# Performance work log

Measured on AMD Instinct MI355X. Metric: run time of the kernel, lower is better.

The kernel has to match this reference:

```python
import jax, jax.numpy as jnp
import numpy as np

N, E, D_IN, D_OUT = 100000, 3200000, 128, 128


def setup_inputs() -> dict:
    key = jax.random.key(0)
    ks = jax.random.split(key, 6)
    return {
        "x": jax.random.normal(ks[0], (N, D_IN), dtype=jnp.float32),
        "row": jax.random.randint(ks[1], (E,), 0, N),
        "col": jax.random.randint(ks[2], (E,), 0, N),
        "W0": jax.random.normal(ks[3], (D_OUT, D_IN), dtype=jnp.float32) * (1.0 / np.sqrt(D_IN)),
        "b0": jnp.zeros((D_OUT,), jnp.float32),
        "W1": jax.random.normal(ks[4], (D_OUT, D_IN), dtype=jnp.float32) * (1.0 / np.sqrt(D_IN)),
        "b1": jnp.zeros((D_OUT,), jnp.float32),
        "att": jax.random.normal(ks[5], (2 * D_OUT,), dtype=jnp.float32) * 0.1,
        "scale0": jnp.ones((D_OUT,), jnp.float32),
        "offset0": jnp.zeros((D_OUT,), jnp.float32),
        "scale1": jnp.ones((D_OUT,), jnp.float32),
        "offset1": jnp.zeros((D_OUT,), jnp.float32),
    }


def _norm(f, scale, offset):
    # per-node normalization over feature dim (bias='norm' branch)
    m = jnp.mean(f, axis=1, keepdims=True)
    v = jnp.var(f, axis=1, keepdims=True) + 1e-9
    return (f - m) * scale * jax.lax.rsqrt(v) + offset


def reference(x, row, col, W0, b0, W1, b1, att, scale0, offset0, scale1, offset1):
    d = W0.shape[0]
    # order-0 (self) and order-1 (neighbor) feature transforms, act='relu'
    h0 = jax.nn.relu(x @ W0.T + b0)  # [N, d]
    h1 = jax.nn.relu(x @ W1.T + b1)  # [N, d]
    # unnormalized GAT attention (no softmax), LeakyReLU(0.2)
    a_self = jax.nn.leaky_relu(h0 @ att[:d], negative_slope=0.2)   # [N]
    a_neigh = jax.nn.leaky_relu(h1 @ att[d:], negative_slope=0.2)  # [N]
    e = a_self[row] + a_neigh[col]                                 # [E]
    # SpMM: out[i] = sum_{(i,j) in edges} e_ij * h1[j]
    agg = jax.ops.segment_sum(e[:, None] * h1[col], row, num_segments=h0.shape[0])
    # batch-norm style normalization per head, then mean-aggregate over orders
    out = _norm(h0, scale0, offset0) + _norm(agg, scale1, offset1)
    return out
```

## Files before the change

### kernel.cpp

```cpp
#include <hip/hip_runtime.h>
#include <hip/hip_bf16.h>

constexpr int D = 128;
constexpr int BUCKET_SHIFT = 6;
constexpr int BUCKET_CAP_LOG2 = 12;
constexpr int BUCKET_CAP = 1 << BUCKET_CAP_LOG2;
constexpr int SEG_SHIFT = 13;
constexpr int NSEG = 13;
constexpr int BINS_PER_BUCKET = 4 * NSEG * 16;
constexpr int BINS_PER_WAVE = NSEG * 16;
constexpr int ROWSTRIDE = 130;
typedef __hip_bfloat16 bf16;
typedef __attribute__((ext_vector_type(8))) short bf16x8;
typedef __attribute__((ext_vector_type(4))) float f32x4;

__device__ __forceinline__ short f2b(float f) {
  bf16 h = __float2bfloat16(f);
  return *reinterpret_cast<short*>(&h);
}

__global__ void k_cvtW(const float* __restrict__ W0, const float* __restrict__ W1,
                       short* __restrict__ Wb0, short* __restrict__ Wb1)
{
  int i = blockIdx.x * 256 + threadIdx.x;
  if (i < 16384) Wb0[i] = f2b(W0[i]);
  else if (i < 32768) { int j = i - 16384; Wb1[j] = f2b(W1[j]); }
}

__global__ __launch_bounds__(256) void k_gemm(
    const float* __restrict__ x,
    const short* __restrict__ Wb0, const float* __restrict__ b0,
    const short* __restrict__ Wb1, const float* __restrict__ b1,
    const float* __restrict__ att,
    float* __restrict__ h0, bf16* __restrict__ h1b,
    float* __restrict__ a_self, float* __restrict__ a_neigh, int N)
{
  const int t = threadIdx.x;
  const int wv = t >> 6;
  const int l = t & 63;
  const int fb = blockIdx.y;
  const int nbase = blockIdx.x * 64 + wv * 16;
  const int lm = l & 15;
  const int lk = l >> 4;

  const short* __restrict__ W    = fb ? Wb1 : Wb0;
  const float* __restrict__ bias = fb ? b1 : b0;
  const float* __restrict__ attp = att + fb * 128;

  f32x4 acc[8];
#pragma unroll
  for (int i = 0; i < 8; ++i) acc[i] = (f32x4){0.f, 0.f, 0.f, 0.f};

  const int node_a = nbase + lm;
  const bool okA = node_a < N;
  const float* xrow = x + (size_t)node_a * D + lk * 8;

#pragma unroll
  for (int ks = 0; ks < 4; ++ks) {
    float4 a0, a1;
    if (okA) {
      a0 = *reinterpret_cast<const float4*>(xrow + ks * 32);
      a1 = *reinterpret_cast<const float4*>(xrow + ks * 32 + 4);
    } else {
      a0 = make_float4(0.f, 0.f, 0.f, 0.f);
      a1 = a0;
    }
    bf16x8 af;
    af[0] = f2b(a0.x); af[1] = f2b(a0.y); af[2] = f2b(a0.z); af[3] = f2b(a0.w);
    af[4] = f2b(a1.x); af[5] = f2b(a1.y); af[6] = f2b(a1.z); af[7] = f2b(a1.w);
#pragma unroll
    for (int nt = 0; nt < 8; ++nt) {
      const bf16x8 bfr = *reinterpret_cast<const bf16x8*>(
          W + (size_t)(nt * 16 + lm) * D + ks * 32 + lk * 8);
      acc[nt] = __builtin_amdgcn_mfma_f32_16x16x32_bf16(af, bfr, acc[nt], 0, 0, 0);
    }
  }

  float pd[4] = {0.f, 0.f, 0.f, 0.f};
#pragma unroll
  for (int nt = 0; nt < 8; ++nt) {
    const int f = nt * 16 + lm;
    const float bv = bias[f];
    const float av = attp[f];
#pragma unroll
    for (int j = 0; j < 4; ++j) {
      const float r = fmaxf(acc[nt][j] + bv, 0.f);
      pd[j] = fmaf(r, av, pd[j]);
      const int ng = nbase + lk * 4 + j;
      if (ng < N) {
        if (fb == 0) h0[(size_t)ng * D + f] = r;
        else         h1b[(size_t)ng * D + f] = __float2bfloat16(r);
      }
    }
  }
#pragma unroll
  for (int m2 = 1; m2 < 16; m2 <<= 1) {
    pd[0] += __shfl_xor(pd[0], m2, 16);
    pd[1] += __shfl_xor(pd[1], m2, 16);
    pd[2] += __shfl_xor(pd[2], m2, 16);
    pd[3] += __shfl_xor(pd[3], m2, 16);
  }
  if (lm == 0) {
    float* __restrict__ adest = fb ? a_neigh : a_self;
#pragma unroll
    for (int j = 0; j < 4; ++j) {
      const int ng = nbase + lk * 4 + j;
      if (ng < N) adest[ng] = pd[j];
    }
  }
}

__global__ __launch_bounds__(512) void k_binA(
    const int* __restrict__ row, const int* __restrict__ col,
    int* __restrict__ bukCnt, unsigned* __restrict__ buf1, int E, int NBUK)
{
  constexpr int EPB = 16384;
  __shared__ int hist[1600];
  __shared__ int base[1600];
  const int t = threadIdx.x;
  const int e0 = blockIdx.x * EPB;
  const int e1 = min(e0 + EPB, E);

  for (int i = t; i < NBUK; i += 512) hist[i] = 0;
  __syncthreads();
  for (int e = e0 + t; e < e1; e += 512)
    atomicAdd(&hist[row[e] >> BUCKET_SHIFT], 1);
  __syncthreads();
  for (int bk = t; bk < NBUK; bk += 512) {
    int c = hist[bk];
    base[bk] = (c > 0) ? atomicAdd(&bukCnt[bk], c) : 0;
  }
  __syncthreads();
  for (int i = t; i < NBUK; i += 512) hist[i] = 0;
  __syncthreads();
  for (int e = e0 + t; e < e1; e += 512) {
    int r = row[e];
    int c = col[e];
    int bk = r >> BUCKET_SHIFT;
    int pos = base[bk] + atomicAdd(&hist[bk], 1);
    if (pos < BUCKET_CAP)
      buf1[((size_t)bk << BUCKET_CAP_LOG2) + pos] =
          ((unsigned)c << BUCKET_SHIFT) | (unsigned)(r & 63);
  }
}

__global__ __launch_bounds__(256) void k_fine(
    const unsigned* __restrict__ buf1,
    const int* __restrict__ bukCnt,
    const float* __restrict__ a_self, const float* __restrict__ a_neigh,
    int* __restrict__ runsW, int2* __restrict__ colS2, int N)
{
  __shared__ int lhist[BINS_PER_BUCKET], labs[BINS_PER_BUCKET], lcur[BINS_PER_BUCKET];
  __shared__ unsigned eL[BUCKET_CAP];
  __shared__ float asF[64];
  __shared__ int sd[256];
  __shared__ int gbS;
  const int b = blockIdx.x;
  const int t = threadIdx.x;
  const int n = min(bukCnt[b], BUCKET_CAP);
  const unsigned* src = buf1 + ((size_t)b << BUCKET_CAP_LOG2);
  const int rstart = b << BUCKET_SHIFT;

  int pre = 0;
  for (int i = t; i < b; i += 256) pre += min(bukCnt[i], BUCKET_CAP);
  sd[t] = pre;
  __syncthreads();
  for (int d2 = 128; d2 > 0; d2 >>= 1) {
    if (t < d2) sd[t] += sd[t + d2];
    __syncthreads();
  }
  if (t == 0) gbS = sd[0];

  for (int i = t; i < BINS_PER_BUCKET; i += 256) { lhist[i] = 0; lcur[i] = 0; }
  if (t < 64) {
    float v = (rstart + t < N) ? a_self[rstart + t] : 0.f;
    asF[t] = v > 0.f ? v : 0.2f * v;
  }
  __syncthreads();
  const int gb = gbS;

  for (int i = t; i < n; i += 256) {
    unsigned e = src[i];
    eL[i] = e;
    int r = e & 63, c = e >> BUCKET_SHIFT;
    int bin = (((r >> 4) * NSEG) + (c >> SEG_SHIFT)) * 16 + (r & 15);
    atomicAdd(&lhist[bin], 1);
  }
  __syncthreads();
  int v[4], s = 0;
  const int bin0 = t * 4;
#pragma unroll
  for (int i = 0; i < 4; ++i) {
    v[i] = (bin0 + i < BINS_PER_BUCKET) ? lhist[bin0 + i] : 0;
    s += v[i];
  }
  sd[t] = s;
  __syncthreads();
  for (int d2 = 1; d2 < 256; d2 <<= 1) {
    int o = (t >= d2) ? sd[t - d2] : 0;
    __syncthreads();
    sd[t] += o;
    __syncthreads();
  }
  int excl = sd[t] - s;
#pragma unroll
  for (int i = 0; i < 4; ++i) {
    if (bin0 + i < BINS_PER_BUCKET) labs[bin0 + i] = gb + excl;
    excl += v[i];
  }
  __syncthreads();
  if (t < 4) runsW[b * 5 + t] = labs[t * BINS_PER_WAVE];
  else if (t == 4) runsW[b * 5 + 4] = gb + n;
  for (int i = t; i < n; i += 256) {
    unsigned e = eL[i];
    int r = e & 63, c = e >> BUCKET_SHIFT;
    int bin = (((r >> 4) * NSEG) + (c >> SEG_SHIFT)) * 16 + (r & 15);
    int pos = labs[bin] + atomicAdd(&lcur[bin], 1);
    float an = a_neigh[c];
    an = an > 0.f ? an : 0.2f * an;
    colS2[pos] = make_int2((c << 8) | r, __float_as_int(asF[r] + an));
  }
}

__global__ __launch_bounds__(128) void k_agg(
    const float* __restrict__ h0, const bf16* __restrict__ h1b,
    const int* __restrict__ runsW, const int2* __restrict__ colS2,
    const float* __restrict__ scale0, const float* __restrict__ offset0,
    const float* __restrict__ scale1, const float* __restrict__ offset1,
    float* __restrict__ out, int N)
{
  __shared__ float aggL[32 * ROWSTRIDE];
  __shared__ int wb[3];
  const int b2 = blockIdx.x;
  const int bk = b2 >> 1, h = b2 & 1;
  const int t = threadIdx.x;
  const int w = t >> 6, l = t & 63;
  const int rbase = (bk << 6) + (h << 5);

  for (int i = t; i < 32 * ROWSTRIDE; i += 128) aggL[i] = 0.f;
  if (t < 3) wb[t] = runsW[bk * 5 + h * 2 + t];
  __syncthreads();

  const char* h1c = reinterpret_cast<const char*>(h1b) + l * 4;
  float acc0 = 0.f, acc1 = 0.f;
  int curRow = -1;

  auto flush = [&]() {
    float* pp = &aggL[(curRow & 31) * ROWSTRIDE + 2 * l];
    const float2 o = *reinterpret_cast<const float2*>(pp);
    *reinterpret_cast<float2*>(pp) = make_float2(o.x + acc0, o.y + acc1);
  };
  auto proc = [&](int2 q, unsigned u) {
    const int r_ = q.x & 63;
    if (r_ != curRow) {
      if (curRow >= 0) flush();
      acc0 = 0.f; acc1 = 0.f; curRow = r_;
    }
    const float wg = __int_as_float(q.y);
    acc0 = fmaf(wg, __uint_as_float(u << 16), acc0);
    acc1 = fmaf(wg, __uint_as_float(u & 0xffff0000u), acc1);
  };
  auto ld = [&](int2 q) -> unsigned {
    return *reinterpret_cast<const unsigned*>(
        h1c + (size_t)((unsigned)q.x & 0xFFFFFF00u));
  };

  const int wbeg = __builtin_amdgcn_readfirstlane(wb[w]);
  const int wend = __builtin_amdgcn_readfirstlane(wb[w + 1]);

  int k = wbeg;
  for (; k + 16 <= wend; k += 16) {
    int2 q[16]; unsigned u[16];
#pragma unroll
    for (int i = 0; i < 16; ++i) q[i] = colS2[k + i];
#pragma unroll
    for (int i = 0; i < 16; ++i) u[i] = ld(q[i]);
#pragma unroll
    for (int i = 0; i < 16; ++i) proc(q[i], u[i]);
  }
  for (; k + 4 <= wend; k += 4) {
    int2 q[4]; unsigned u[4];
#pragma unroll
    for (int i = 0; i < 4; ++i) q[i] = colS2[k + i];
#pragma unroll
    for (int i = 0; i < 4; ++i) u[i] = ld(q[i]);
#pragma unroll
    for (int i = 0; i < 4; ++i) proc(q[i], u[i]);
  }
  for (; k < wend; ++k) {
    const int2 q = colS2[k];
    proc(q, ld(q));
  }
  if (curRow >= 0) flush();
  __syncthreads();

  const float2 sc0 = *reinterpret_cast<const float2*>(&scale0[2 * l]);
  const float2 of0 = *reinterpret_cast<const float2*>(&offset0[2 * l]);
  const float2 sc1 = *reinterpret_cast<const float2*>(&scale1[2 * l]);
  const float2 of1 = *reinterpret_cast<const float2*>(&offset1[2 * l]);
  const float inv = 1.0f / 128.0f;
  for (int i = 0; i < 16; ++i) {
    const int rl = (w << 4) + i;
    const int node = rbase + rl;
    if (node >= N) break;
    const float2 hv = *reinterpret_cast<const float2*>(&h0[(size_t)node * D + 2 * l]);
    const float2 av = *reinterpret_cast<const float2*>(&aggL[rl * ROWSTRIDE + 2 * l]);
    float sh = hv.x + hv.y, qh = hv.x * hv.x + hv.y * hv.y;
    float sa = av.x + av.y, qa = av.x * av.x + av.y * av.y;
#pragma unroll
    for (int o = 32; o; o >>= 1) {
      sh += __shfl_xor(sh, o, 64); qh += __shfl_xor(qh, o, 64);
      sa += __shfl_xor(sa, o, 64); qa += __shfl_xor(qa, o, 64);
    }
    const float m0 = sh * inv, v0 = qh * inv - m0 * m0 + 1e-9f;
    const float m1 = sa * inv, v1 = qa * inv - m1 * m1 + 1e-9f;
    const float r0 = rsqrtf(v0), r1 = rsqrtf(v1);
    float2 o2;
    o2.x = (hv.x - m0) * sc0.x * r0 + of0.x + (av.x - m1) * sc1.x * r1 + of1.x;
    o2.y = (hv.y - m0) * sc0.y * r0 + of0.y + (av.y - m1) * sc1.y * r1 + of1.y;
    *reinterpret_cast<float2*>(&out[(size_t)node * D + 2 * l]) = o2;
  }
}

extern "C" void kernel_launch(void* const* d_in, const int* in_sizes, int n_in,
                              void* d_out, int out_size, void* d_ws, size_t ws_size,
                              hipStream_t stream)
{
  const float* x       = (const float*)d_in[0];
  const int*   row     = (const int*)d_in[1];
  const int*   col     = (const int*)d_in[2];
  const float* W0      = (const float*)d_in[3];
  const float* b0      = (const float*)d_in[4];
  const float* W1      = (const float*)d_in[5];
  const float* b1      = (const float*)d_in[6];
  const float* att     = (const float*)d_in[7];
  const float* scale0  = (const float*)d_in[8];
  const float* offset0 = (const float*)d_in[9];
  const float* scale1  = (const float*)d_in[10];
  const float* offset1 = (const float*)d_in[11];

  const int N = in_sizes[0] / D;
  const int E = in_sizes[1];
  const int NBUK = (N + 63) >> BUCKET_SHIFT;

  char* ws = (char*)d_ws;
  size_t off = 0;
  auto alloc = [&](size_t bytes) -> void* {
    void* p = ws + off;
    off += (bytes + 511) & ~size_t(511);
    return p;
  };

  float*    h0      = (float*)d_out;
  bf16*     h1b     = (bf16*)alloc((size_t)N * D * sizeof(bf16));
  float*    a_self  = (float*)alloc((size_t)N * sizeof(float));
  float*    a_neigh = (float*)alloc((size_t)N * sizeof(float));
  short*    Wb0     = (short*)alloc(16384 * sizeof(short));
  short*    Wb1     = (short*)alloc(16384 * sizeof(short));
  int*      bukCnt  = (int*)alloc((size_t)NBUK * sizeof(int));
  int*      runsW   = (int*)alloc((size_t)NBUK * 5 * sizeof(int));
  unsigned* buf1    = (unsigned*)alloc(((size_t)NBUK << BUCKET_CAP_LOG2) * sizeof(unsigned));
  int2*     colS2   = (int2*)alloc((size_t)E * sizeof(int2));

  hipMemsetAsync(bukCnt, 0, (size_t)NBUK * sizeof(int), stream);

  k_cvtW<<<128, 256, 0, stream>>>(W0, W1, Wb0, Wb1);
  dim3 ggrid((N + 63) / 64, 2);
  k_gemm<<<ggrid, 256, 0, stream>>>(x, Wb0, b0, Wb1, b1, att, h0, h1b,
                                    a_self, a_neigh, N);
  const int NBLKA = (E + 16383) / 16384;
  k_binA<<<NBLKA, 512, 0, stream>>>(row, col, bukCnt, buf1, E, NBUK);
  k_fine<<<NBUK, 256, 0, stream>>>(buf1, bukCnt, a_self, a_neigh,
                                   runsW, colS2, N);
  k_agg<<<NBUK * 2, 128, 0, stream>>>(h0, h1b, runsW, colS2,
                                      scale0, offset0, scale1, offset1,
                                      (float*)d_out, N);
}
```

Baseline: 280.2 us.

## Fuse GEMM and edge-binning into one launch, inline weight bf16 conversion

```diff
diff --git a/kernel.cpp b/kernel.cpp
--- a/kernel.cpp
+++ b/kernel.cpp
@@ -10,6 +10,7 @@
 constexpr int BINS_PER_BUCKET = 4 * NSEG * 16;
 constexpr int BINS_PER_WAVE = NSEG * 16;
 constexpr int ROWSTRIDE = 130;
+constexpr int EPB_BIN = 8192;
 typedef __hip_bfloat16 bf16;
 typedef __attribute__((ext_vector_type(8))) short bf16x8;
 typedef __attribute__((ext_vector_type(4))) float f32x4;
@@ -19,128 +20,125 @@
   return *reinterpret_cast<short*>(&h);
 }
 
-__global__ void k_cvtW(const float* __restrict__ W0, const float* __restrict__ W1,
-                       short* __restrict__ Wb0, short* __restrict__ Wb1)
-{
-  int i = blockIdx.x * 256 + threadIdx.x;
-  if (i < 16384) Wb0[i] = f2b(W0[i]);
-  else if (i < 32768) { int j = i - 16384; Wb1[j] = f2b(W1[j]); }
-}
-
-__global__ __launch_bounds__(256) void k_gemm(
+__global__ __launch_bounds__(256) void k_gb(
     const float* __restrict__ x,
-    const short* __restrict__ Wb0, const float* __restrict__ b0,
-    const short* __restrict__ Wb1, const float* __restrict__ b1,
+    const float* __restrict__ W0, const float* __restrict__ b0,
+    const float* __restrict__ W1, const float* __restrict__ b1,
     const float* __restrict__ att,
     float* __restrict__ h0, bf16* __restrict__ h1b,
-    float* __restrict__ a_self, float* __restrict__ a_neigh, int N)
+    float* __restrict__ a_self, float* __restrict__ a_neigh,
+    const int* __restrict__ row, const int* __restrict__ col,
+    int* __restrict__ bukCnt, unsigned* __restrict__ buf1,
+    int N, int E, int NBUK, int NBLKA)
 {
+  __shared__ int sm[3200];
   const int t = threadIdx.x;
-  const int wv = t >> 6;
-  const int l = t & 63;
-  const int fb = blockIdx.y;
-  const int nbase = blockIdx.x * 64 + wv * 16;
-  const int lm = l & 15;
-  const int lk = l >> 4;
-
-  const short* __restrict__ W    = fb ? Wb1 : Wb0;
-  const float* __restrict__ bias = fb ? b1 : b0;
-  const float* __restrict__ attp = att + fb * 128;
-
-  f32x4 acc[8];
-#pragma unroll
-  for (int i = 0; i < 8; ++i) acc[i] = (f32x4){0.f, 0.f, 0.f, 0.f};
-
-  const int node_a = nbase + lm;
-  const bool okA = node_a < N;
-  const float* xrow = x + (size_t)node_a * D + lk * 8;
-
-#pragma unroll
-  for (int ks = 0; ks < 4; ++ks) {
-    float4 a0, a1;
-    if (okA) {
-      a0 = *reinterpret_cast<const float4*>(xrow + ks * 32);
-      a1 = *reinterpret_cast<const float4*>(xrow + ks * 32 + 4);
-    } else {
-      a0 = make_float4(0.f, 0.f, 0.f, 0.f);
-      a1 = a0;
-    }
-    bf16x8 af;
-    af[0] = f2b(a0.x); af[1] = f2b(a0.y); af[2] = f2b(a0.z); af[3] = f2b(a0.w);
-    af[4] = f2b(a1.x); af[5] = f2b(a1.y); af[6] = f2b(a1.z); af[7] = f2b(a1.w);
+
+  if (blockIdx.y < 2) {
+    const int wv = t >> 6;
+    const int l = t & 63;
+    const int fb = blockIdx.y;
+    const int nbase = blockIdx.x * 64 + wv * 16;
+    const int lm = l & 15;
+    const int lk = l >> 4;
+
+    const float* __restrict__ W    = fb ? W1 : W0;
+    const float* __restrict__ bias = fb ? b1 : b0;
+    const float* __restrict__ attp = att + fb * 128;
+
+    f32x4 acc[8];
+#pragma unroll
+    for (int i = 0; i < 8; ++i) acc[i] = (f32x4){0.f, 0.f, 0.f, 0.f};
+
+    const int node_a = nbase + lm;
+    const bool okA = node_a < N;
+    const float* xrow = x + (size_t)node_a * D + lk * 8;
+
+#pragma unroll
+    for (int ks = 0; ks < 4; ++ks) {
+      float4 a0, a1;
+      if (okA) {
+        a0 = *reinterpret_cast<const float4*>(xrow + ks * 32);
+        a1 = *reinterpret_cast<const float4*>(xrow + ks * 32 + 4);
+      } else {
+        a0 = make_float4(0.f, 0.f, 0.f, 0.f);
+        a1 = a0;
+      }
+      bf16x8 af;
+      af[0] = f2b(a0.x); af[1] = f2b(a0.y); af[2] = f2b(a0.z); af[3] = f2b(a0.w);
+      af[4] = f2b(a1.x); af[5] = f2b(a1.y); af[6] = f2b(a1.z); af[7] = f2b(a1.w);
+#pragma unroll
+      for (int nt = 0; nt < 8; ++nt) {
+        const float* wr = W + (size_t)(nt * 16 + lm) * D + ks * 32 + lk * 8;
+        const float4 w0 = *reinterpret_cast<const float4*>(wr);
+        const float4 w1 = *reinterpret_cast<const float4*>(wr + 4);
+        bf16x8 bfr;
+        bfr[0] = f2b(w0.x); bfr[1] = f2b(w0.y); bfr[2] = f2b(w0.z); bfr[3] = f2b(w0.w);
+        bfr[4] = f2b(w1.x); bfr[5] = f2b(w1.y); bfr[6] = f2b(w1.z); bfr[7] = f2b(w1.w);
+        acc[nt] = __builtin_amdgcn_mfma_f32_16x16x32_bf16(af, bfr, acc[nt], 0, 0, 0);
+      }
+    }
+
+    float pd[4] = {0.f, 0.f, 0.f, 0.f};
 #pragma unroll
     for (int nt = 0; nt < 8; ++nt) {
-      const bf16x8 bfr = *reinterpret_cast<const bf16x8*>(
-          W + (size_t)(nt * 16 + lm) * D + ks * 32 + lk * 8);
-      acc[nt] = __builtin_amdgcn_mfma_f32_16x16x32_bf16(af, bfr, acc[nt], 0, 0, 0);
-    }
-  }
-
-  float pd[4] = {0.f, 0.f, 0.f, 0.f};
-#pragma unroll
-  for (int nt = 0; nt < 8; ++nt) {
-    const int f = nt * 16 + lm;
-    const float bv = bias[f];
-    const float av = attp[f];
-#pragma unroll
-    for (int j = 0; j < 4; ++j) {
-      const float r = fmaxf(acc[nt][j] + bv, 0.f);
-      pd[j] = fmaf(r, av, pd[j]);
-      const int ng = nbase + lk * 4 + j;
-      if (ng < N) {
-        if (fb == 0) h0[(size_t)ng * D + f] = r;
-        else         h1b[(size_t)ng * D + f] = __float2bfloat16(r);
+      const int f = nt * 16 + lm;
+      const float bv = bias[f];
+      const float av = attp[f];
+#pragma unroll
+      for (int j = 0; j < 4; ++j) {
+        const float r = fmaxf(acc[nt][j] + bv, 0.f);
+        pd[j] = fmaf(r, av, pd[j]);
+        const int ng = nbase + lk * 4 + j;
+        if (ng < N) {
+          if (fb == 0) h0[(size_t)ng * D + f] = r;
+          else         h1b[(size_t)ng * D + f] = __float2bfloat16(r);
+        }
       }
     }
-  }
-#pragma unroll
-  for (int m2 = 1; m2 < 16; m2 <<= 1) {
-    pd[0] += __shfl_xor(pd[0], m2, 16);
-    pd[1] += __shfl_xor(pd[1], m2, 16);
-    pd[2] += __shfl_xor(pd[2], m2, 16);
-    pd[3] += __shfl_xor(pd[3], m2, 16);
-  }
-  if (lm == 0) {
-    float* __restrict__ adest = fb ? a_neigh : a_self;
-#pragma unroll
-    for (int j = 0; j < 4; ++j) {
-      const int ng = nbase + lk * 4 + j;
-      if (ng < N) adest[ng] = pd[j];
-    }
-  }
-}
-
-__global__ __launch_bounds__(512) void k_binA(
-    const int* __restrict__ row, const int* __restrict__ col,
-    int* __restrict__ bukCnt, unsigned* __restrict__ buf1, int E, int NBUK)
-{
-  constexpr int EPB = 16384;
-  __shared__ int hist[1600];
-  __shared__ int base[1600];
-  const int t = threadIdx.x;
-  const int e0 = blockIdx.x * EPB;
-  const int e1 = min(e0 + EPB, E);
-
-  for (int i = t; i < NBUK; i += 512) hist[i] = 0;
-  __syncthreads();
-  for (int e = e0 + t; e < e1; e += 512)
-    atomicAdd(&hist[row[e] >> BUCKET_SHIFT], 1);
-  __syncthreads();
-  for (int bk = t; bk < NBUK; bk += 512) {
-    int c = hist[bk];
-    base[bk] = (c > 0) ? atomicAdd(&bukCnt[bk], c) : 0;
-  }
-  __syncthreads();
-  for (int i = t; i < NBUK; i += 512) hist[i] = 0;
-  __syncthreads();
-  for (int e = e0 + t; e < e1; e += 512) {
-    int r = row[e];
-    int c = col[e];
-    int bk = r >> BUCKET_SHIFT;
-    int pos = base[bk] + atomicAdd(&hist[bk], 1);
-    if (pos < BUCKET_CAP)
-      buf1[((size_t)bk << BUCKET_CAP_LOG2) + pos] =
-          ((unsigned)c << BUCKET_SHIFT) | (unsigned)(r & 63);
+#pragma unroll
+    for (int m2 = 1; m2 < 16; m2 <<= 1) {
+      pd[0] += __shfl_xor(pd[0], m2, 16);
+      pd[1] += __shfl_xor(pd[1], m2, 16);
+      pd[2] += __shfl_xor(pd[2], m2, 16);
+      pd[3] += __shfl_xor(pd[3], m2, 16);
+    }
+    if (lm == 0) {
+      float* __restrict__ adest = fb ? a_neigh : a_self;
+#pragma unroll
+      for (int j = 0; j < 4; ++j) {
+        const int ng = nbase + lk * 4 + j;
+        if (ng < N) adest[ng] = pd[j];
+      }
+    }
+  } else {
+    if (blockIdx.x >= NBLKA) return;
+    int* hist = sm;
+    int* base = sm + 1600;
+    const int e0 = blockIdx.x * EPB_BIN;
+    const int e1 = min(e0 + EPB_BIN, E);
+
+    for (int i = t; i < NBUK; i += 256) hist[i] = 0;
+    __syncthreads();
+    for (int e = e0 + t; e < e1; e += 256)
+      atomicAdd(&hist[row[e] >> BUCKET_SHIFT], 1);
+    __syncthreads();
+    for (int bk = t; bk < NBUK; bk += 256) {
+      int c = hist[bk];
+      base[bk] = (c > 0) ? atomicAdd(&bukCnt[bk], c) : 0;
+    }
+    __syncthreads();
+    for (int i = t; i < NBUK; i += 256) hist[i] = 0;
+    __syncthreads();
+    for (int e = e0 + t; e < e1; e += 256) {
+      int r = row[e];
+      int c = col[e];
+      int bk = r >> BUCKET_SHIFT;
+      int pos = base[bk] + atomicAdd(&hist[bk], 1);
+      if (pos < BUCKET_CAP)
+        buf1[((size_t)bk << BUCKET_CAP_LOG2) + pos] =
+            ((unsigned)c << BUCKET_SHIFT) | (unsigned)(r & 63);
+    }
   }
 }
 
@@ -342,6 +340,7 @@
   const int N = in_sizes[0] / D;
   const int E = in_sizes[1];
   const int NBUK = (N + 63) >> BUCKET_SHIFT;
+  const int NBLKA = (E + EPB_BIN - 1) / EPB_BIN;
 
   char* ws = (char*)d_ws;
   size_t off = 0;
@@ -355,8 +354,6 @@
   bf16*     h1b     = (bf16*)alloc((size_t)N * D * sizeof(bf16));
   float*    a_self  = (float*)alloc((size_t)N * sizeof(float));
   float*    a_neigh = (float*)alloc((size_t)N * sizeof(float));
-  short*    Wb0     = (short*)alloc(16384 * sizeof(short));
-  short*    Wb1     = (short*)alloc(16384 * sizeof(short));
   int*      bukCnt  = (int*)alloc((size_t)NBUK * sizeof(int));
   int*      runsW   = (int*)alloc((size_t)NBUK * 5 * sizeof(int));
   unsigned* buf1    = (unsigned*)alloc(((size_t)NBUK << BUCKET_CAP_LOG2) * sizeof(unsigned));
@@ -364,12 +361,10 @@
 
   hipMemsetAsync(bukCnt, 0, (size_t)NBUK * sizeof(int), stream);
 
-  k_cvtW<<<128, 256, 0, stream>>>(W0, W1, Wb0, Wb1);
-  dim3 ggrid((N + 63) / 64, 2);
-  k_gemm<<<ggrid, 256, 0, stream>>>(x, Wb0, b0, Wb1, b1, att, h0, h1b,
-                                    a_self, a_neigh, N);
-  const int NBLKA = (E + 16383) / 16384;
-  k_binA<<<NBLKA, 512, 0, stream>>>(row, col, bukCnt, buf1, E, NBUK);
+  dim3 ggrid((N + 63) / 64, 3);
+  k_gb<<<ggrid, 256, 0, stream>>>(x, W0, b0, W1, b1, att, h0, h1b,
+                                  a_self, a_neigh, row, col, bukCnt, buf1,
+                                  N, E, NBUK, NBLKA);
   k_fine<<<NBUK, 256, 0, stream>>>(buf1, bukCnt, a_self, a_neigh,
                                    runsW, colS2, N);
   k_agg<<<NBUK * 2, 128, 0, stream>>>(h0, h1b, runsW, colS2,
```

Result: slower. 312.8 us (+11.6%).
